# Performance work log

Hardware: AMD Instinct MI355X
Metric: run time of the kernel (lower is better)

Reference implementation:

```python
import jax, jax.numpy as jnp
import numpy as np

B, T, N = 512, 512, 128   # batch, timesteps, driving series
M = 64                    # LSTM hidden size
UNITS = 64                # attention units


def setup_inputs() -> dict:
    key = jax.random.key(0)
    ks = jax.random.split(key, 9)
    s = lambda fan_in: 1.0 / np.sqrt(fan_in)
    return {
        "x": jax.random.normal(ks[0], (B, T, N), jnp.float32),
        "hidden_state": jax.random.normal(ks[1], (B, M), jnp.float32),
        "cell_state": jax.random.normal(ks[2], (B, M), jnp.float32),
        # Dense(units) applied to x permuted to (B, N, T): kernel contracts T
        "w1_kernel": jax.random.normal(ks[3], (T, UNITS), jnp.float32) * s(T),
        "w1_bias": jnp.zeros((UNITS,), jnp.float32),
        # Dense(units) applied to query (B, N, 2M)
        "w2_kernel": jax.random.normal(ks[4], (2 * M, UNITS), jnp.float32) * s(2 * M),
        "w2_bias": jnp.zeros((UNITS,), jnp.float32),
        # Dense(1) scoring
        "v_kernel": jax.random.normal(ks[5], (UNITS, 1), jnp.float32) * s(UNITS),
        "v_bias": jnp.zeros((1,), jnp.float32),
    }


def reference(x, hidden_state, cell_state, w1_kernel, w1_bias,
              w2_kernel, w2_bias, v_kernel, v_bias):
    # query: (B, 2M) -> broadcast over the N feature axis (RepeatVector)
    query = jnp.concatenate([hidden_state, cell_state], axis=-1)
    q_proj = query @ w2_kernel + w2_bias                    # (B, UNITS)
    x_perm = jnp.transpose(x, (0, 2, 1))                    # (B, N, T)
    score = jnp.tanh(x_perm @ w1_kernel + w1_bias + q_proj[:, None, :])  # (B, N, UNITS)
    score = score @ v_kernel + v_bias                       # (B, N, 1)
    score = jnp.transpose(score, (0, 2, 1))                 # (B, 1, N)
    attention_weights = jax.nn.softmax(score, axis=-1)      # (B, 1, N)
    context_vector = jnp.sum(attention_weights * x, axis=-1)  # (B, T)
    return context_vector, attention_weights
```

## Files before the change

kernel.cpp:

```cpp
#include <hip/hip_runtime.h>
#include <hip/hip_bf16.h>

namespace {

constexpr int kB = 512, kT = 512, kN = 128, kM = 64, kU = 64;
constexpr int WST = 72;
constexpr int XST = 520;
constexpr int RST = 12;
constexpr int CST = 528;

typedef __attribute__((ext_vector_type(8))) short short8;
typedef __attribute__((ext_vector_type(16))) float f32x16;

__device__ __forceinline__ unsigned rne16(float v) {
  unsigned u = __float_as_uint(v);
  return (u + 0x7fffu + ((u >> 16) & 1u)) >> 16;
}
__device__ __forceinline__ float fb16(unsigned h) { return __uint_as_float(h << 16); }

__device__ __forceinline__ unsigned pack_hl(float v) {
  unsigned h = rne16(v);
  unsigned l = rne16(v - fb16(h));
  return (h << 16) | (l & 0xffffu);
}

__device__ __forceinline__ float fast_tanh(float x) {
  return 1.0f - 2.0f / (__expf(2.0f * x) + 1.0f);
}

union FragU { unsigned u[4]; short8 s; };

__device__ __forceinline__ void unpack_hl(const unsigned* p, short8& hi, short8& lo) {
  FragU H, L;
#pragma unroll
  for (int j = 0; j < 4; ++j) {
    unsigned a = p[2 * j], b = p[2 * j + 1];
    H.u[j] = (a >> 16) | (b & 0xffff0000u);
    L.u[j] = (a & 0xffffu) | (b << 16);
  }
  hi = H.s; lo = L.s;
}

__device__ __forceinline__ void pack8(const float* v, short8& hi, short8& lo) {
  FragU H, L;
#pragma unroll
  for (int jj = 0; jj < 4; ++jj) {
    float v0 = v[2 * jj], v1 = v[2 * jj + 1];
    unsigned h0 = rne16(v0), h1 = rne16(v1);
    unsigned l0 = rne16(v0 - fb16(h0)), l1 = rne16(v1 - fb16(h1));
    H.u[jj] = h0 | (h1 << 16);
    L.u[jj] = l0 | (l1 << 16);
  }
  hi = H.s; lo = L.s;
}

struct Smem {
  union {
    unsigned wstage[kU * WST];
    float red[256 * RST];
    float red2[8 * CST];
  } u;
  unsigned short xbf[kN * XST];
  float qpart[8][kU];
  float qpfull[kU];
  float sn[kN];
  float aw[kN];
};

__global__ __launch_bounds__(512, 2) void fused_kernel(
    const float* __restrict__ x,
    const float* __restrict__ hs,
    const float* __restrict__ cs,
    const float* __restrict__ w1,
    const float* __restrict__ w1b,
    const float* __restrict__ w2,
    const float* __restrict__ w2b,
    const float* __restrict__ vk,
    float* __restrict__ ctx_out,
    float* __restrict__ aw_out)
{
  extern __shared__ char smem_raw[];
  Smem& s = *reinterpret_cast<Smem*>(smem_raw);

  const int b = blockIdx.x;
  const int tid = threadIdx.x;
  const int l = tid & 63;
  const int w = tid >> 6;
  const int g = w >> 2;
  const int m = w & 3;
  const int ln = l & 31;
  const int kh = l >> 5;
  const int nA = 32 * m + ln;

  {
    const int u = tid & 63, kg = tid >> 6;
    float a0 = 0.f;
#pragma unroll
    for (int j = 0; j < 16; ++j) {
      int k = kg * 16 + j;
      float qv = (k < kM) ? hs[(size_t)b * kM + k] : cs[(size_t)b * kM + (k - kM)];
      a0 = fmaf(qv, w2[k * kU + u], a0);
    }
    s.qpart[kg][u] = a0;
  }

  f32x16 acc0, acc1;
#pragma unroll
  for (int i = 0; i < 16; ++i) { acc0[i] = 0.f; acc1[i] = 0.f; }

  for (int sub = 0; sub < 8; ++sub) {
    const int tb = g * 256 + sub * 32;
    __syncthreads();

    float rA[2][8];
#pragma unroll
    for (int ks = 0; ks < 2; ++ks)
#pragma unroll
      for (int j = 0; j < 8; ++j)
        rA[ks][j] = x[((size_t)b * kT + tb + ks * 16 + 8 * kh + j) * kN + nA];

#pragma unroll
    for (int i = 0; i < 8; ++i) {
      int idx = tid + i * 512;
      int u = idx & 63, tr = idx >> 6;
      int gg = tr >> 5, lt = tr & 31;
      float v = w1[(size_t)(gg * 256 + sub * 32 + lt) * kU + u];
      s.u.wstage[u * WST + 36 * gg + (lt ^ ((u & 7) << 2))] = pack_hl(v);
    }
    __syncthreads();

#pragma unroll
    for (int ks = 0; ks < 2; ++ks) {
      short8 ah, al;
      pack8(rA[ks], ah, al);
      const int tcur = tb + ks * 16 + 8 * kh;
      *(short8*)&s.xbf[nA * XST + tcur] = ah;
      const int ltk = ks * 16 + 8 * kh;
#pragma unroll
      for (int ut = 0; ut < 2; ++ut) {
        const int u = 32 * ut + ln;
        const int sw = (u & 7) << 2;
        const unsigned* base = &s.u.wstage[u * WST + 36 * g];
        unsigned rb[8];
        *(uint4*)&rb[0] = *(const uint4*)&base[ltk ^ sw];
        *(uint4*)&rb[4] = *(const uint4*)&base[(ltk + 4) ^ sw];
        short8 bh, bl;
        unpack_hl(rb, bh, bl);
        f32x16& a = ut ? acc1 : acc0;
        a = __builtin_amdgcn_mfma_f32_32x32x16_bf16(ah, bh, a, 0, 0, 0);
        a = __builtin_amdgcn_mfma_f32_32x32x16_bf16(ah, bl, a, 0, 0, 0);
        a = __builtin_amdgcn_mfma_f32_32x32x16_bf16(al, bh, a, 0, 0, 0);
      }
    }
  }
  __syncthreads();

  const int rrow = ((w & 3) * 64 + l) * RST;
#pragma unroll
  for (int rnd = 0; rnd < 4; ++rnd) {
    f32x16& a = (rnd < 2) ? acc0 : acc1;
    const int off = (rnd & 1) * 8;
    if (g == 1) {
#pragma unroll
      for (int j = 0; j < 8; ++j) s.u.red[rrow + j] = a[off + j];
    }
    __syncthreads();
    if (g == 0) {
#pragma unroll
      for (int j = 0; j < 8; ++j) a[off + j] += s.u.red[rrow + j];
    }
    __syncthreads();
  }

  if (tid < kU) {
    float v = w2b[tid] + w1b[tid];
#pragma unroll
    for (int gg = 0; gg < 8; ++gg) v += s.qpart[gg][tid];
    s.qpfull[tid] = v;
  }
  __syncthreads();

  if (g == 0) {
    const float qp0 = s.qpfull[ln], qp1 = s.qpfull[32 + ln];
    const float v0 = vk[ln], v1 = vk[32 + ln];
    float pr[16];
#pragma unroll
    for (int r = 0; r < 16; ++r)
      pr[r] = fmaf(fast_tanh(acc0[r] + qp0), v0, fast_tanh(acc1[r] + qp1) * v1);
#pragma unroll
    for (int off = 1; off < 32; off <<= 1)
#pragma unroll
      for (int r = 0; r < 16; ++r)
        pr[r] += __shfl_xor(pr[r], off);
    if (ln == 0) {
#pragma unroll
      for (int r = 0; r < 16; ++r)
        s.sn[32 * m + (r & 3) + 8 * (r >> 2) + 4 * kh] = pr[r];
    }
  }
  __syncthreads();

  if (tid < 64) {
    float s0 = s.sn[tid], s1 = s.sn[tid + 64];
    float mx = fmaxf(s0, s1);
#pragma unroll
    for (int off = 32; off > 0; off >>= 1) mx = fmaxf(mx, __shfl_xor(mx, off));
    float e0 = __expf(s0 - mx), e1 = __expf(s1 - mx);
    float se = e0 + e1;
#pragma unroll
    for (int off = 32; off > 0; off >>= 1) se += __shfl_xor(se, off);
    float inv = 1.0f / se;
    float a0 = e0 * inv, a1 = e1 * inv;
    s.aw[tid] = a0;
    s.aw[tid + 64] = a1;
    aw_out[(size_t)b * kN + tid] = a0;
    aw_out[(size_t)b * kN + tid + 64] = a1;
  }
  __syncthreads();

  {
    float cp[8];
#pragma unroll
    for (int j = 0; j < 8; ++j) cp[j] = 0.f;
    const int nb = 16 * w;
#pragma unroll
    for (int nn = 0; nn < 16; ++nn) {
      const int n = nb + nn;
      const float a = s.aw[n];
      short8 xv = *(const short8*)&s.xbf[n * XST + 8 * l];
#pragma unroll
      for (int j = 0; j < 8; ++j)
        cp[j] = fmaf(fb16((unsigned)(unsigned short)xv[j]), a, cp[j]);
    }
    float4 c0 = {cp[0], cp[1], cp[2], cp[3]};
    float4 c1 = {cp[4], cp[5], cp[6], cp[7]};
    *(float4*)&s.u.red2[w * CST + 8 * l] = c0;
    *(float4*)&s.u.red2[w * CST + 8 * l + 4] = c1;
  }
  __syncthreads();
  {
    float c = 0.f;
#pragma unroll
    for (int ww = 0; ww < 8; ++ww) c += s.u.red2[ww * CST + tid];
    ctx_out[(size_t)b * kT + tid] = c;
  }
}

}

extern "C" void kernel_launch(void* const* d_in, const int* in_sizes, int n_in,
                              void* d_out, int out_size, void* d_ws, size_t ws_size,
                              hipStream_t stream) {
  const float* x   = (const float*)d_in[0];
  const float* hs  = (const float*)d_in[1];
  const float* cs  = (const float*)d_in[2];
  const float* w1  = (const float*)d_in[3];
  const float* w1b = (const float*)d_in[4];
  const float* w2  = (const float*)d_in[5];
  const float* w2b = (const float*)d_in[6];
  const float* vk  = (const float*)d_in[7];

  float* out = (float*)d_out;
  float* ctx = out;
  float* awo = out + (size_t)kB * kT;

  static_assert(sizeof(Smem) <= 160 * 1024, "LDS overflow");
  (void)hipFuncSetAttribute(reinterpret_cast<const void*>(fused_kernel),
                            hipFuncAttributeMaxDynamicSharedMemorySize,
                            (int)sizeof(Smem));
  hipLaunchKernelGGL(fused_kernel, dim3(kB), dim3(512), sizeof(Smem), stream,
                     x, hs, cs, w1, w1b, w2, w2b, vk, ctx, awo);
}
```

Before: 221.2 us.

## Prepack W1 into workspace and double-buffer global loads in the MFMA loop

A small prep kernel converts w1 into packed bf16 hi/lo pairs once per call, laid out so each lane can load its B fragment straight from global memory. The fused kernel drops the per-subtile LDS staging of W1 and its two barriers per iteration, and software-pipelines the x and weight loads two subtiles ahead. This removes repeated pack work and sync stalls. The cost is an extra launch, a workspace buffer, higher register pressure from two in-flight buffers, and more global or L2 traffic for the weights.

```diff
diff --git a/kernel.cpp b/kernel.cpp
--- a/kernel.cpp
+++ b/kernel.cpp
@@ -4,7 +4,6 @@
 namespace {
 
 constexpr int kB = 512, kT = 512, kN = 128, kM = 64, kU = 64;
-constexpr int WST = 72;
 constexpr int XST = 520;
 constexpr int RST = 12;
 constexpr int CST = 528;
@@ -56,7 +55,6 @@
 
 struct Smem {
   union {
-    unsigned wstage[kU * WST];
     float red[256 * RST];
     float red2[8 * CST];
   } u;
@@ -67,11 +65,18 @@
   float aw[kN];
 };
 
+__global__ __launch_bounds__(512) void prep_w1(const float* __restrict__ w1,
+                                               unsigned* __restrict__ pw) {
+  const int gid = blockIdx.x * blockDim.x + threadIdx.x;
+  const int t = gid >> 6, u = gid & 63;
+  pw[(((t >> 3) * 64 + u) << 3) | (t & 7)] = pack_hl(w1[gid]);
+}
+
 __global__ __launch_bounds__(512, 2) void fused_kernel(
     const float* __restrict__ x,
     const float* __restrict__ hs,
     const float* __restrict__ cs,
-    const float* __restrict__ w1,
+    const unsigned* __restrict__ pw,
     const float* __restrict__ w1b,
     const float* __restrict__ w2,
     const float* __restrict__ w2b,
@@ -108,51 +113,60 @@
 #pragma unroll
   for (int i = 0; i < 16; ++i) { acc0[i] = 0.f; acc1[i] = 0.f; }
 
-  for (int sub = 0; sub < 8; ++sub) {
+  const float* xb = x + (size_t)b * kT * kN;
+
+  struct SubBuf { float rA[2][8]; uint4 rb[2][2][2]; };
+
+  auto issue = [&](SubBuf& bf, int sub) {
     const int tb = g * 256 + sub * 32;
-    __syncthreads();
-
-    float rA[2][8];
-#pragma unroll
-    for (int ks = 0; ks < 2; ++ks)
+#pragma unroll
+    for (int ks = 0; ks < 2; ++ks) {
+      const int t0 = tb + ks * 16 + 8 * kh;
 #pragma unroll
       for (int j = 0; j < 8; ++j)
-        rA[ks][j] = x[((size_t)b * kT + tb + ks * 16 + 8 * kh + j) * kN + nA];
-
-#pragma unroll
-    for (int i = 0; i < 8; ++i) {
-      int idx = tid + i * 512;
-      int u = idx & 63, tr = idx >> 6;
-      int gg = tr >> 5, lt = tr & 31;
-      float v = w1[(size_t)(gg * 256 + sub * 32 + lt) * kU + u];
-      s.u.wstage[u * WST + 36 * gg + (lt ^ ((u & 7) << 2))] = pack_hl(v);
-    }
-    __syncthreads();
-
+        bf.rA[ks][j] = xb[(size_t)(t0 + j) * kN + nA];
+#pragma unroll
+      for (int ut = 0; ut < 2; ++ut) {
+        const int base = ((t0 >> 3) * 64 + 32 * ut + ln) * 8;
+        bf.rb[ks][ut][0] = *(const uint4*)&pw[base];
+        bf.rb[ks][ut][1] = *(const uint4*)&pw[base + 4];
+      }
+    }
+  };
+
+  auto compute = [&](SubBuf& bf, int sub) {
+    const int tb = g * 256 + sub * 32;
 #pragma unroll
     for (int ks = 0; ks < 2; ++ks) {
       short8 ah, al;
-      pack8(rA[ks], ah, al);
+      pack8(bf.rA[ks], ah, al);
       const int tcur = tb + ks * 16 + 8 * kh;
       *(short8*)&s.xbf[nA * XST + tcur] = ah;
-      const int ltk = ks * 16 + 8 * kh;
 #pragma unroll
       for (int ut = 0; ut < 2; ++ut) {
-        const int u = 32 * ut + ln;
-        const int sw = (u & 7) << 2;
-        const unsigned* base = &s.u.wstage[u * WST + 36 * g];
-        unsigned rb[8];
-        *(uint4*)&rb[0] = *(const uint4*)&base[ltk ^ sw];
-        *(uint4*)&rb[4] = *(const uint4*)&base[(ltk + 4) ^ sw];
         short8 bh, bl;
-        unpack_hl(rb, bh, bl);
+        unpack_hl((const unsigned*)&bf.rb[ks][ut][0], bh, bl);
         f32x16& a = ut ? acc1 : acc0;
         a = __builtin_amdgcn_mfma_f32_32x32x16_bf16(ah, bh, a, 0, 0, 0);
         a = __builtin_amdgcn_mfma_f32_32x32x16_bf16(ah, bl, a, 0, 0, 0);
         a = __builtin_amdgcn_mfma_f32_32x32x16_bf16(al, bh, a, 0, 0, 0);
       }
     }
-  }
+  };
+
+  {
+    SubBuf A_, B_;
+    issue(A_, 0);
+    issue(B_, 1);
+#pragma unroll
+    for (int s2 = 0; s2 < 8; s2 += 2) {
+      compute(A_, s2);
+      if (s2 + 2 < 8) issue(A_, s2 + 2);
+      compute(B_, s2 + 1);
+      if (s2 + 3 < 8) issue(B_, s2 + 3);
+    }
+  }
+
   __syncthreads();
 
   const int rrow = ((w & 3) * 64 + l) * RST;
@@ -264,10 +278,13 @@
   float* ctx = out;
   float* awo = out + (size_t)kB * kT;
 
+  unsigned* pw = (unsigned*)d_ws;
+
   static_assert(sizeof(Smem) <= 160 * 1024, "LDS overflow");
   (void)hipFuncSetAttribute(reinterpret_cast<const void*>(fused_kernel),
                             hipFuncAttributeMaxDynamicSharedMemorySize,
                             (int)sizeof(Smem));
+  hipLaunchKernelGGL(prep_w1, dim3(64), dim3(512), 0, stream, w1, pw);
   hipLaunchKernelGGL(fused_kernel, dim3(kB), dim3(512), sizeof(Smem), stream,
-                     x, hs, cs, w1, w1b, w2, w2b, vk, ctx, awo);
-}
+                     x, hs, cs, pw, w1b, w2, w2b, vk, ctx, awo);
+}
```

Result: no change. 218.5 us (-1.2%).
